# Kernel optimization log

Measured on AMD Instinct MI355X. Metric: run time of the kernel, lower is better.

The kernel has to match this reference:

```python
import jax, jax.numpy as jnp
import numpy as np

C = 64          # number of concepts (output_size)
MC = 100        # num_monte_carlo
TRI = C * (C + 1) // 2
ROWS, COLS = np.tril_indices(C)          # static lower-triangular indices
DIAG_MASK = ROWS == COLS                 # positions in c_sigma that are diagonal
DIAG = np.arange(C)


def setup_inputs() -> dict:
    key = jax.random.key(0)
    k_x, k_eps, k_wmu, k_wsig = jax.random.split(key, 4)
    B, F = 4096, 512
    return {
        "x": jax.random.normal(k_x, (B, F), jnp.float32),
        "eps": jax.random.normal(k_eps, (B, C, MC), jnp.float32),  # MVN standard-normal draws
        "w_mu": jax.random.normal(k_wmu, (C, F), jnp.float32) / np.float32(np.sqrt(F)),
        "b_mu": jnp.zeros((C,), jnp.float32),
        # sigma.weight.data *= 0.01 in the original module
        "w_sigma": jax.random.normal(k_wsig, (TRI, F), jnp.float32) * np.float32(0.01 / np.sqrt(F)),
        "b_sigma": jnp.zeros((TRI,), jnp.float32),
    }


def reference(x, eps, w_mu, b_mu, w_sigma, b_sigma):
    # mu head: Linear(F -> C)
    c_mu = x @ w_mu.T + b_mu                          # [B, C]
    # sigma head: Linear(F -> C*(C+1)/2)
    c_sigma = x @ w_sigma.T + b_sigma                 # [B, TRI]

    B = x.shape[0]
    # build lower-triangular scale matrix (predict_sigma)
    L = jnp.zeros((B, C, C), x.dtype)
    L = L.at[:, ROWS, COLS].set(c_sigma)
    diag_vals = jax.nn.softplus(c_sigma[:, DIAG_MASK]) + 1e-6
    L = L.at[:, DIAG, DIAG].set(diag_vals)            # [B, C, C]

    # MVN rsample([MC]) with scale_tril L: sample = mu + L @ eps
    logits = c_mu[:, :, None] + jnp.einsum('bij,bjm->bim', L, eps)  # [B, C, MC]
    return jax.nn.sigmoid(logits)
```

## Files before the change

### kernel.cpp

```cpp
#include <hip/hip_runtime.h>
#include <hip/hip_bf16.h>


typedef short bf16x8 __attribute__((ext_vector_type(8)));
typedef float f32x4 __attribute__((ext_vector_type(4)));

__device__ __forceinline__ unsigned short f2bf(float f) {
    union { float f; unsigned u; } u; u.f = f;
    unsigned r = u.u + 0x7FFFu + ((u.u >> 16) & 1u);
    return (unsigned short)(r >> 16);
}

__device__ __forceinline__ int swz(int r) { return (r ^ (r >> 3)) & 7; }

__device__ __forceinline__ void tri_ij(int t, int& i, int& j) {
    i = (int)((sqrtf((float)(8 * t + 1)) - 1.0f) * 0.5f);
    if ((i + 1) * (i + 2) / 2 <= t) ++i;
    if (i * (i + 1) / 2 > t) --i;
    j = t - ((i * (i + 1)) >> 1);
}

__device__ __forceinline__ void gload16(const void* g, void* l) {
    __builtin_amdgcn_global_load_lds(
        (const __attribute__((address_space(1))) void*)g,
        (__attribute__((address_space(3))) void*)l, 16, 0, 0);
}

__global__ __launch_bounds__(256) void cvt_kernel(
    const float* __restrict__ x, const float* __restrict__ wmu,
    const float* __restrict__ wsig,
    unsigned short* __restrict__ Xb, unsigned short* __restrict__ Wb) {
    const int NX = (4096 * 512) / 4;
    const int NW = (2144 * 512) / 4;
    const int NMU = (64 * 512) / 4;
    int tot = NX + NW;
    for (int i = blockIdx.x * blockDim.x + threadIdx.x; i < tot;
         i += gridDim.x * blockDim.x) {
        float4 v; unsigned short* dst;
        if (i < NX) {
            v = ((const float4*)x)[i];
            dst = Xb + (size_t)i * 4;
        } else {
            int j = i - NX;
            if (j < NMU) v = ((const float4*)wmu)[j];
            else         v = ((const float4*)wsig)[j - NMU];
            dst = Wb + (size_t)j * 4;
        }
        ushort4 o;
        o.x = f2bf(v.x); o.y = f2bf(v.y); o.z = f2bf(v.z); o.w = f2bf(v.w);
        *(ushort4*)dst = o;
    }
}

__global__ __launch_bounds__(256) void gemm_kernel(
    const unsigned short* __restrict__ Xb, const unsigned short* __restrict__ Wb,
    const float* __restrict__ bmu, const float* __restrict__ bsig,
    float* __restrict__ Mu, unsigned short* __restrict__ Sg) {
    __shared__ __align__(16) unsigned short smem[16384];

    int flat = blockIdx.y * 17 + blockIdx.x;
    int virt = (flat & 7) * 68 + (flat >> 3);
    int vbx = virt % 17, vby = virt / 17;
    int r0 = vby * 128, c0 = vbx * 128;

    int tid = threadIdx.x;
    int w = tid >> 6, lane = tid & 63;
    int wr = w >> 1, wc = w & 1;
    int lr = lane & 15, kg = lane >> 4;

    int sr = tid >> 3;
    int sc = tid & 7;
    int scx = sc ^ (sr & 7);
    const unsigned short* Ag = Xb + (size_t)(r0 + sr) * 512 + scx * 8;
    const unsigned short* Bg = Wb + (size_t)(c0 + sr) * 512 + scx * 8;
    unsigned short* As = smem + tid * 8;
    unsigned short* Bs = smem + 8192 + tid * 8;

    f32x4 acc[4][4];
    #pragma unroll
    for (int i = 0; i < 4; ++i)
        #pragma unroll
        for (int j = 0; j < 4; ++j) acc[i][j] = (f32x4){0.f, 0.f, 0.f, 0.f};

    for (int kt = 0; kt < 8; ++kt) {
        int k0 = kt * 64;
        #pragma unroll
        for (int i = 0; i < 4; ++i) {
            gload16(Ag + (size_t)i * 32 * 512 + k0, As + i * 2048);
            gload16(Bg + (size_t)i * 32 * 512 + k0, Bs + i * 2048);
        }
        __syncthreads();
        #pragma unroll
        for (int h = 0; h < 2; ++h) {
            bf16x8 a[4], bv[4];
            #pragma unroll
            for (int i = 0; i < 4; ++i) {
                int row = wr * 64 + i * 16 + lr;
                int ch = ((h << 2) | kg) ^ (row & 7);
                a[i] = *(const bf16x8*)(smem + row * 64 + ch * 8);
            }
            #pragma unroll
            for (int j = 0; j < 4; ++j) {
                int row = wc * 64 + j * 16 + lr;
                int ch = ((h << 2) | kg) ^ (row & 7);
                bv[j] = *(const bf16x8*)(smem + 8192 + row * 64 + ch * 8);
            }
            #pragma unroll
            for (int i = 0; i < 4; ++i)
                #pragma unroll
                for (int j = 0; j < 4; ++j)
                    acc[i][j] = __builtin_amdgcn_mfma_f32_16x16x32_bf16(
                        a[i], bv[j], acc[i][j], 0, 0, 0);
        }
        __syncthreads();
    }

    int rbase = r0 + wr * 64 + (kg << 2);
    #pragma unroll
    for (int j = 0; j < 4; ++j) {
        int col = c0 + wc * 64 + j * 16 + lr;
        if (col < 64) {
            float bias = bmu[col];
            #pragma unroll
            for (int i = 0; i < 4; ++i)
                #pragma unroll
                for (int r = 0; r < 4; ++r)
                    Mu[(size_t)(rbase + i * 16 + r) * 64 + col] = acc[i][j][r] + bias;
        } else if (col < 2144) {
            int t = col - 64;
            float bias = bsig[t];
            int ti, tj; tri_ij(t, ti, tj);
            bool dg = (tj == ti);
            #pragma unroll
            for (int i = 0; i < 4; ++i) {
                #pragma unroll
                for (int r = 0; r < 4; ++r) {
                    float v = acc[i][j][r] + bias;
                    if (dg) v = (v > 15.f ? v : __logf(1.f + __expf(v))) + 1e-6f;
                    Sg[(size_t)(rbase + i * 16 + r) * 2080 + t] = f2bf(v);
                }
            }
        }
    }
}

__global__ __launch_bounds__(512, 8) void sample_kernel(
    const float* __restrict__ Mu, const unsigned short* __restrict__ Sg,
    const float* __restrict__ eps, float* __restrict__ out) {
    __shared__ __align__(16) unsigned short Lh[64][64];
    __shared__ __align__(16) float Ost[64][128];

    int b = blockIdx.x;
    int tid = threadIdx.x;
    int w = tid >> 6;
    int lane = tid & 63;
    int lr = lane & 15, kg = lane >> 4;
    const float* er = eps + (size_t)b * 6400;

    float ef[16];
    int m = (w << 4) + lr;
    int ml = (m < 100) ? m : 96;
    if (w < 7) {
        #pragma unroll
        for (int s = 0; s < 8; ++s) {
            ef[s]     = er[(kg * 8 + s) * 100 + ml];
            ef[s + 8] = er[(32 + kg * 8 + s) * 100 + ml];
        }
    }

    const unsigned short* sgu = Sg + (size_t)b * 2080;
    #pragma unroll
    for (int k = 0; k < 4; ++k) {
        int idx = tid + (k << 9);
        int i = idx >> 5;
        int j0 = (idx & 31) << 1;
        unsigned u = 0u;
        if (j0 <= i) {
            int t = ((i * (i + 1)) >> 1) + j0;
            u = sgu[t];
            if (j0 + 1 <= i) u |= ((unsigned)sgu[t + 1]) << 16;
        }
        *(unsigned*)&Lh[i][(((j0 >> 3) ^ swz(i)) << 3) | (j0 & 7)] = u;
    }

    float muv[4];
    bf16x8 a0, a1;
    if (w < 7) {
        #pragma unroll
        for (int g = 0; g < 4; ++g) muv[g] = Mu[(b << 6) + g * 16 + lr];
        #pragma unroll
        for (int s = 0; s < 4; ++s) {
            __hip_bfloat162 h0 = __float22bfloat162_rn(
                make_float2(ef[2 * s], ef[2 * s + 1]));
            __hip_bfloat162 h1 = __float22bfloat162_rn(
                make_float2(ef[8 + 2 * s], ef[8 + 2 * s + 1]));
            ((unsigned*)&a0)[s] = *(unsigned*)&h0;
            ((unsigned*)&a1)[s] = *(unsigned*)&h1;
        }
    }

    __syncthreads();

    if (w < 7) {
        int m0 = (w << 4) + (kg << 2);
        #pragma unroll
        for (int g = 0; g < 4; ++g) {
            int i = g * 16 + lr;
            int si = swz(i);
            bf16x8 L0 = *(const bf16x8*)&Lh[i][(kg ^ si) << 3];
            bf16x8 L1 = *(const bf16x8*)&Lh[i][((kg + 4) ^ si) << 3];
            f32x4 acc = {0.f, 0.f, 0.f, 0.f};
            acc = __builtin_amdgcn_mfma_f32_16x16x32_bf16(a0, L0, acc, 0, 0, 0);
            acc = __builtin_amdgcn_mfma_f32_16x16x32_bf16(a1, L1, acc, 0, 0, 0);
            if (m0 < 100) {
                float4 o;
                #pragma unroll
                for (int r = 0; r < 4; ++r) {
                    float z = muv[g] + acc[r];
                    ((float*)&o)[r] = __fdividef(1.f, 1.f + __expf(-z));
                }
                *(float4*)&Ost[i][m0 ^ ((i & 7) << 2)] = o;
            }
        }
    }

    __syncthreads();

    #pragma unroll
    for (int k = 0; k < 4; ++k) {
        int f = tid + (k << 9);
        if (f < 1600) {
            int row = f / 25;
            int c4 = (f % 25) << 2;
            float4 v = *(const float4*)&Ost[row][c4 ^ ((row & 7) << 2)];
            *(float4*)(out + ((size_t)b * 64 + row) * 100 + c4) = v;
        }
    }
}

extern "C" void kernel_launch(void* const* d_in, const int* in_sizes, int n_in,
                              void* d_out, int out_size, void* d_ws, size_t ws_size,
                              hipStream_t stream) {
    const float* x    = (const float*)d_in[0];
    const float* eps  = (const float*)d_in[1];
    const float* wmu  = (const float*)d_in[2];
    const float* bmu  = (const float*)d_in[3];
    const float* wsig = (const float*)d_in[4];
    const float* bsig = (const float*)d_in[5];
    float* out = (float*)d_out;

    char* ws = (char*)d_ws;
    unsigned short* Xb = (unsigned short*)ws;
    unsigned short* Wb = (unsigned short*)(ws + 4194304);
    float*          Mu = (float*)(ws + 4194304 + 2195456);
    unsigned short* Sg = (unsigned short*)(ws + 4194304 + 2195456 + 1048576);

    cvt_kernel<<<2048, 256, 0, stream>>>(x, wmu, wsig, Xb, Wb);
    gemm_kernel<<<dim3(17, 32), 256, 0, stream>>>(Xb, Wb, bmu, bsig, Mu, Sg);
    sample_kernel<<<4096, 512, 0, stream>>>(Mu, Sg, eps, out);
}
```

Measured before the change: 77.50 us.

## Pipeline sample kernel over four batches per block with double-buffered LDS

The sample kernel now handles four batch rows per block (1024 blocks instead of 4096). It prefetches the next row's sigma triangle into LDS asynchronously and loads its eps and mu into registers while the current row's MFMA runs, which should hide load latency. It also drops the LDS output staging and writes float4 results straight to global memory, with a remapped block index for locality. In exchange the direct stores are less coalesced (rows of 100 floats written in 4-float pieces by lane), there are fewer blocks to fill the GPU, and register pressure rises.

```diff
diff --git a/kernel.cpp b/kernel.cpp
--- a/kernel.cpp
+++ b/kernel.cpp
@@ -147,94 +147,104 @@
 __global__ __launch_bounds__(512, 8) void sample_kernel(
     const float* __restrict__ Mu, const unsigned short* __restrict__ Sg,
     const float* __restrict__ eps, float* __restrict__ out) {
-    __shared__ __align__(16) unsigned short Lh[64][64];
-    __shared__ __align__(16) float Ost[64][128];
-
-    int b = blockIdx.x;
+    __shared__ __align__(16) unsigned short raw[2][2080];
+    __shared__ __align__(16) unsigned short Lh[2][64][64];
+
+    int flat = blockIdx.x;
+    int virt = (flat & 7) * 128 + (flat >> 3);
+    int b0 = virt << 2;
+
     int tid = threadIdx.x;
-    int w = tid >> 6;
-    int lane = tid & 63;
+    int w = tid >> 6, lane = tid & 63;
     int lr = lane & 15, kg = lane >> 4;
-    const float* er = eps + (size_t)b * 6400;
-
-    float ef[16];
     int m = (w << 4) + lr;
     int ml = (m < 100) ? m : 96;
-    if (w < 7) {
-        #pragma unroll
-        for (int s = 0; s < 8; ++s) {
-            ef[s]     = er[(kg * 8 + s) * 100 + ml];
-            ef[s + 8] = er[(32 + kg * 8 + s) * 100 + ml];
-        }
-    }
-
-    const unsigned short* sgu = Sg + (size_t)b * 2080;
+    int m0 = (w << 4) + (kg << 2);
+    bool cw = (w < 7);
+    bool st = cw && (m0 < 100);
+
+    if (tid < 260)
+        gload16(Sg + (size_t)b0 * 2080 + tid * 8, &raw[0][tid * 8]);
+
+    float ef[16], mun[4], muc[4];
+    bf16x8 a0, a1;
+
+    __syncthreads();
+
     #pragma unroll
-    for (int k = 0; k < 4; ++k) {
-        int idx = tid + (k << 9);
-        int i = idx >> 5;
-        int j0 = (idx & 31) << 1;
-        unsigned u = 0u;
-        if (j0 <= i) {
-            int t = ((i * (i + 1)) >> 1) + j0;
-            u = sgu[t];
-            if (j0 + 1 <= i) u |= ((unsigned)sgu[t + 1]) << 16;
-        }
-        *(unsigned*)&Lh[i][(((j0 >> 3) ^ swz(i)) << 3) | (j0 & 7)] = u;
-    }
-
-    float muv[4];
-    bf16x8 a0, a1;
-    if (w < 7) {
-        #pragma unroll
-        for (int g = 0; g < 4; ++g) muv[g] = Mu[(b << 6) + g * 16 + lr];
-        #pragma unroll
-        for (int s = 0; s < 4; ++s) {
-            __hip_bfloat162 h0 = __float22bfloat162_rn(
-                make_float2(ef[2 * s], ef[2 * s + 1]));
-            __hip_bfloat162 h1 = __float22bfloat162_rn(
-                make_float2(ef[8 + 2 * s], ef[8 + 2 * s + 1]));
-            ((unsigned*)&a0)[s] = *(unsigned*)&h0;
-            ((unsigned*)&a1)[s] = *(unsigned*)&h1;
-        }
-    }
-
-    __syncthreads();
-
-    if (w < 7) {
-        int m0 = (w << 4) + (kg << 2);
-        #pragma unroll
-        for (int g = 0; g < 4; ++g) {
-            int i = g * 16 + lr;
-            int si = swz(i);
-            bf16x8 L0 = *(const bf16x8*)&Lh[i][(kg ^ si) << 3];
-            bf16x8 L1 = *(const bf16x8*)&Lh[i][((kg + 4) ^ si) << 3];
-            f32x4 acc = {0.f, 0.f, 0.f, 0.f};
-            acc = __builtin_amdgcn_mfma_f32_16x16x32_bf16(a0, L0, acc, 0, 0, 0);
-            acc = __builtin_amdgcn_mfma_f32_16x16x32_bf16(a1, L1, acc, 0, 0, 0);
-            if (m0 < 100) {
-                float4 o;
-                #pragma unroll
-                for (int r = 0; r < 4; ++r) {
-                    float z = muv[g] + acc[r];
-                    ((float*)&o)[r] = __fdividef(1.f, 1.f + __expf(-z));
+    for (int it = 0; it <= 4; ++it) {
+        int b = b0 + it;
+        int cur = it & 1;
+
+        if (it >= 1 && cw) {
+            #pragma unroll
+            for (int s = 0; s < 4; ++s) {
+                __hip_bfloat162 h0 = __float22bfloat162_rn(
+                    make_float2(ef[2 * s], ef[2 * s + 1]));
+                __hip_bfloat162 h1 = __float22bfloat162_rn(
+                    make_float2(ef[8 + 2 * s], ef[8 + 2 * s + 1]));
+                ((unsigned*)&a0)[s] = *(unsigned*)&h0;
+                ((unsigned*)&a1)[s] = *(unsigned*)&h1;
+            }
+            #pragma unroll
+            for (int g = 0; g < 4; ++g) muc[g] = mun[g];
+        }
+
+        if (it <= 3 && cw) {
+            const float* er = eps + (size_t)b * 6400;
+            #pragma unroll
+            for (int s = 0; s < 8; ++s) {
+                ef[s]     = er[(kg * 8 + s) * 100 + ml];
+                ef[s + 8] = er[(32 + kg * 8 + s) * 100 + ml];
+            }
+            #pragma unroll
+            for (int g = 0; g < 4; ++g)
+                mun[g] = Mu[((size_t)b << 6) + g * 16 + lr];
+        }
+
+        if (it <= 2 && tid < 260)
+            gload16(Sg + (size_t)(b + 1) * 2080 + tid * 8, &raw[cur ^ 1][tid * 8]);
+
+        if (it <= 3) {
+            #pragma unroll
+            for (int k = 0; k < 4; ++k) {
+                int idx = tid + (k << 9);
+                int i = idx >> 5;
+                int j0 = (idx & 31) << 1;
+                unsigned u = 0u;
+                if (j0 <= i) {
+                    int t = ((i * (i + 1)) >> 1) + j0;
+                    u = raw[cur][t];
+                    if (j0 + 1 <= i) u |= ((unsigned)raw[cur][t + 1]) << 16;
                 }
-                *(float4*)&Ost[i][m0 ^ ((i & 7) << 2)] = o;
-            }
-        }
-    }
-
-    __syncthreads();
-
-    #pragma unroll
-    for (int k = 0; k < 4; ++k) {
-        int f = tid + (k << 9);
-        if (f < 1600) {
-            int row = f / 25;
-            int c4 = (f % 25) << 2;
-            float4 v = *(const float4*)&Ost[row][c4 ^ ((row & 7) << 2)];
-            *(float4*)(out + ((size_t)b * 64 + row) * 100 + c4) = v;
-        }
+                *(unsigned*)&Lh[cur][i][(((j0 >> 3) ^ swz(i)) << 3) | (j0 & 7)] = u;
+            }
+        }
+
+        if (it >= 1 && cw) {
+            int bp = b - 1;
+            #pragma unroll
+            for (int g = 0; g < 4; ++g) {
+                int i = g * 16 + lr;
+                int si = swz(i);
+                bf16x8 L0 = *(const bf16x8*)&Lh[cur ^ 1][i][(kg ^ si) << 3];
+                bf16x8 L1 = *(const bf16x8*)&Lh[cur ^ 1][i][((kg + 4) ^ si) << 3];
+                f32x4 acc = {0.f, 0.f, 0.f, 0.f};
+                acc = __builtin_amdgcn_mfma_f32_16x16x32_bf16(a0, L0, acc, 0, 0, 0);
+                acc = __builtin_amdgcn_mfma_f32_16x16x32_bf16(a1, L1, acc, 0, 0, 0);
+                if (st) {
+                    float4 o;
+                    #pragma unroll
+                    for (int r = 0; r < 4; ++r) {
+                        float z = muc[g] + acc[r];
+                        ((float*)&o)[r] = __fdividef(1.f, 1.f + __expf(-z));
+                    }
+                    *(float4*)(out + ((size_t)bp * 64 + i) * 100 + m0) = o;
+                }
+            }
+        }
+
+        __syncthreads();
     }
 }
 
@@ -257,5 +267,5 @@
 
     cvt_kernel<<<2048, 256, 0, stream>>>(x, wmu, wsig, Xb, Wb);
     gemm_kernel<<<dim3(17, 32), 256, 0, stream>>>(Xb, Wb, bmu, bsig, Mu, Sg);
-    sample_kernel<<<4096, 512, 0, stream>>>(Mu, Sg, eps, out);
-}
+    sample_kernel<<<1024, 512, 0, stream>>>(Mu, Sg, eps, out);
+}
```

After: 307.2 us. +296.4%, slower.

## Restructure sample kernel: per-wave row tiles with register-resident L, no block barriers

Applied to the files above, without the earlier changes.

Each block now uses 4 waves, and each wave owns 16 rows of L. A wave loads its L fragment straight from global memory into registers, which removes the shared-memory L staging and the first barrier. The wave then loops over all 7 sample tiles, stages its own output rows in a per-wave shared buffer and writes them out without a block-wide sync. The block-to-batch mapping is also permuted, which may help cache or channel locality. The trade-off is many scalar 2-byte global loads for L and 7 serialized eps-load/MFMA iterations per wave instead of spreading that work across waves.

```diff
diff --git a/kernel.cpp b/kernel.cpp
--- a/kernel.cpp
+++ b/kernel.cpp
@@ -10,8 +10,6 @@
     unsigned r = u.u + 0x7FFFu + ((u.u >> 16) & 1u);
     return (unsigned short)(r >> 16);
 }
-
-__device__ __forceinline__ int swz(int r) { return (r ^ (r >> 3)) & 7; }
 
 __device__ __forceinline__ void tri_ij(int t, int& i, int& j) {
     i = (int)((sqrtf((float)(8 * t + 1)) - 1.0f) * 0.5f);
@@ -144,50 +142,49 @@
     }
 }
 
-__global__ __launch_bounds__(512, 8) void sample_kernel(
+__global__ __launch_bounds__(256, 4) void sample_kernel(
     const float* __restrict__ Mu, const unsigned short* __restrict__ Sg,
     const float* __restrict__ eps, float* __restrict__ out) {
-    __shared__ __align__(16) unsigned short Lh[64][64];
-    __shared__ __align__(16) float Ost[64][128];
-
-    int b = blockIdx.x;
+    __shared__ __align__(16) float Ost[4][1600];
+
+    int flat = blockIdx.x;
+    int b = (flat & 7) * 512 + (flat >> 3);
+
     int tid = threadIdx.x;
-    int w = tid >> 6;
-    int lane = tid & 63;
+    int w = tid >> 6, lane = tid & 63;
     int lr = lane & 15, kg = lane >> 4;
+    int i = (w << 4) + lr;
+
+    const unsigned short* sgb = Sg + (size_t)b * 2080;
+    int t0 = (i * (i + 1)) >> 1;
+    bf16x8 L0, L1;
+    #pragma unroll
+    for (int s = 0; s < 4; ++s) {
+        int ja = kg * 8 + 2 * s;
+        int jb = ja + 1;
+        unsigned va = (ja <= i) ? (unsigned)sgb[t0 + ja] : 0u;
+        unsigned vb = (jb <= i) ? (unsigned)sgb[t0 + jb] : 0u;
+        ((unsigned*)&L0)[s] = va | (vb << 16);
+        int jc = ja + 32, jd = jb + 32;
+        unsigned vc = (jc <= i) ? (unsigned)sgb[t0 + jc] : 0u;
+        unsigned vd = (jd <= i) ? (unsigned)sgb[t0 + jd] : 0u;
+        ((unsigned*)&L1)[s] = vc | (vd << 16);
+    }
+
+    float mu = Mu[((size_t)b << 6) + i];
     const float* er = eps + (size_t)b * 6400;
 
-    float ef[16];
-    int m = (w << 4) + lr;
-    int ml = (m < 100) ? m : 96;
-    if (w < 7) {
+    #pragma unroll
+    for (int mt = 0; mt < 7; ++mt) {
+        int m = (mt << 4) + lr;
+        int ml = (m < 100) ? m : 96;
+        float ef[16];
         #pragma unroll
         for (int s = 0; s < 8; ++s) {
             ef[s]     = er[(kg * 8 + s) * 100 + ml];
             ef[s + 8] = er[(32 + kg * 8 + s) * 100 + ml];
         }
-    }
-
-    const unsigned short* sgu = Sg + (size_t)b * 2080;
-    #pragma unroll
-    for (int k = 0; k < 4; ++k) {
-        int idx = tid + (k << 9);
-        int i = idx >> 5;
-        int j0 = (idx & 31) << 1;
-        unsigned u = 0u;
-        if (j0 <= i) {
-            int t = ((i * (i + 1)) >> 1) + j0;
-            u = sgu[t];
-            if (j0 + 1 <= i) u |= ((unsigned)sgu[t + 1]) << 16;
-        }
-        *(unsigned*)&Lh[i][(((j0 >> 3) ^ swz(i)) << 3) | (j0 & 7)] = u;
-    }
-
-    float muv[4];
-    bf16x8 a0, a1;
-    if (w < 7) {
-        #pragma unroll
-        for (int g = 0; g < 4; ++g) muv[g] = Mu[(b << 6) + g * 16 + lr];
+        bf16x8 a0, a1;
         #pragma unroll
         for (int s = 0; s < 4; ++s) {
             __hip_bfloat162 h0 = __float22bfloat162_rn(
@@ -197,44 +194,28 @@
             ((unsigned*)&a0)[s] = *(unsigned*)&h0;
             ((unsigned*)&a1)[s] = *(unsigned*)&h1;
         }
-    }
-
-    __syncthreads();
-
-    if (w < 7) {
-        int m0 = (w << 4) + (kg << 2);
-        #pragma unroll
-        for (int g = 0; g < 4; ++g) {
-            int i = g * 16 + lr;
-            int si = swz(i);
-            bf16x8 L0 = *(const bf16x8*)&Lh[i][(kg ^ si) << 3];
-            bf16x8 L1 = *(const bf16x8*)&Lh[i][((kg + 4) ^ si) << 3];
-            f32x4 acc = {0.f, 0.f, 0.f, 0.f};
-            acc = __builtin_amdgcn_mfma_f32_16x16x32_bf16(a0, L0, acc, 0, 0, 0);
-            acc = __builtin_amdgcn_mfma_f32_16x16x32_bf16(a1, L1, acc, 0, 0, 0);
-            if (m0 < 100) {
-                float4 o;
-                #pragma unroll
-                for (int r = 0; r < 4; ++r) {
-                    float z = muv[g] + acc[r];
-                    ((float*)&o)[r] = __fdividef(1.f, 1.f + __expf(-z));
-                }
-                *(float4*)&Ost[i][m0 ^ ((i & 7) << 2)] = o;
-            }
-        }
-    }
-
-    __syncthreads();
-
-    #pragma unroll
-    for (int k = 0; k < 4; ++k) {
-        int f = tid + (k << 9);
-        if (f < 1600) {
-            int row = f / 25;
-            int c4 = (f % 25) << 2;
-            float4 v = *(const float4*)&Ost[row][c4 ^ ((row & 7) << 2)];
-            *(float4*)(out + ((size_t)b * 64 + row) * 100 + c4) = v;
-        }
+        f32x4 acc = {0.f, 0.f, 0.f, 0.f};
+        acc = __builtin_amdgcn_mfma_f32_16x16x32_bf16(a0, L0, acc, 0, 0, 0);
+        acc = __builtin_amdgcn_mfma_f32_16x16x32_bf16(a1, L1, acc, 0, 0, 0);
+        int m0 = (mt << 4) + (kg << 2);
+        if (m0 < 100) {
+            float4 o;
+            #pragma unroll
+            for (int r = 0; r < 4; ++r) {
+                float z = mu + acc[r];
+                ((float*)&o)[r] = __fdividef(1.f, 1.f + __expf(-z));
+            }
+            *(float4*)&Ost[w][lr * 100 + m0] = o;
+        }
+    }
+
+    float* ob = out + (size_t)b * 6400 + w * 1600;
+    const float4* src = (const float4*)&Ost[w][0];
+    #pragma unroll
+    for (int it = 0; it < 7; ++it) {
+        int f = it * 64 + lane;
+        if (f < 400)
+            ((float4*)ob)[f] = src[f];
     }
 }
 
@@ -257,5 +238,5 @@
 
     cvt_kernel<<<2048, 256, 0, stream>>>(x, wmu, wsig, Xb, Wb);
     gemm_kernel<<<dim3(17, 32), 256, 0, stream>>>(Xb, Wb, bmu, bsig, Mu, Sg);
-    sample_kernel<<<4096, 512, 0, stream>>>(Mu, Sg, eps, out);
-}
+    sample_kernel<<<4096, 256, 0, stream>>>(Mu, Sg, eps, out);
+}
```

Result: slower. 90.06 us (+16.2%).
